# Optimization experiments

Measured on AMD Instinct MI355X. Metric: run time of the kernel, lower is better.

The kernel has to match this reference:

```python
import jax, jax.numpy as jnp
import numpy as np

N = 40000      # nodes (adj.size(0))
ISIZE = 64     # feature dim
K = 24         # kept kNN neighbors per node after d_cut mask
E = N * K      # learner candidate edges
E_ADJ = N * K  # GCN adjacency edges
OMEGA = 0.9
GAMMA = 2.0
D_CUT = 1.5


def setup_inputs() -> dict:
    key = jax.random.key(0)
    k = jax.random.split(key, 8)
    features = jax.random.normal(k[0], (N, ISIZE), jnp.float32)
    sc = 1.0 / np.sqrt(ISIZE)
    W1 = jax.random.normal(k[1], (ISIZE, ISIZE), jnp.float32) * sc
    b1 = jnp.zeros((ISIZE,), jnp.float32)
    W2 = jax.random.normal(k[2], (ISIZE, ISIZE), jnp.float32) * sc
    b2 = jnp.zeros((ISIZE,), jnp.float32)
    adj_row = jax.random.randint(k[3], (E_ADJ,), 0, N, dtype=jnp.int32)
    adj_col = jax.random.randint(k[4], (E_ADJ,), 0, N, dtype=jnp.int32)
    # kNN-style candidate edges: K neighbors per node, no self loops
    i_idx = jnp.repeat(jnp.arange(N, dtype=jnp.int32), K)
    j_idx = (i_idx + jax.random.randint(k[5], (E,), 1, N, dtype=jnp.int32)) % N
    # precomputed distance prior: s_d = 1/exp(gamma*(d/d_cut)^2)
    dist = jax.random.uniform(k[6], (E,), jnp.float32, 0.1, 2.0)
    s_d = jnp.exp(-GAMMA * (dist / D_CUT) ** 2)
    return {"features": features, "W1": W1, "b1": b1, "W2": W2, "b2": b2,
            "s_d": s_d, "adj_row": adj_row, "adj_col": adj_col,
            "i_idx": i_idx, "j_idx": j_idx}


def _gcn(x, W, b, row, col):
    """PyG GCNConv: symmetric norm with self loops, aggregate src=row into dst=col."""
    xw = x @ W
    deg = 1.0 + jax.ops.segment_sum(jnp.ones((row.shape[0],), jnp.float32), col,
                                    num_segments=N)
    dinv = jax.lax.rsqrt(deg)
    msg = (dinv[row] * dinv[col])[:, None] * xw[row]            # [E_ADJ, ISIZE]
    out = jax.ops.segment_sum(msg, col, num_segments=N)
    return out + (dinv * dinv)[:, None] * xw + b                # self-loop + bias


def reference(features, W1, b1, W2, b2, s_d, adj_row, adj_col, i_idx, j_idx):
    # GCN stack (nlayers=2), ReLU between layers
    h = jax.nn.relu(_gcn(features, W1, b1, adj_row, adj_col))
    h = _gcn(h, W2, b2, adj_row, adj_col)
    # F.normalize(h, p=2, dim=-1)
    h = h / jnp.maximum(jnp.linalg.norm(h, axis=-1, keepdims=True), 1e-12)
    # per-edge cosine scores, clamped at 0, blended with distance prior
    s_val = jnp.sum(h[i_idx] * h[j_idx], axis=-1)               # [E]
    s_val = jax.nn.relu(s_val)
    s_val = OMEGA * s_val + (1.0 - OMEGA) * s_d
    # SparseTensor.to_symmetric(reduce='mean'): average with reverse edge if present
    keys = i_idx * N + j_idx                                    # fits int32 (N=4e4)
    rkeys = j_idx * N + i_idx
    order = jnp.argsort(keys)
    sk = keys[order]
    pos = jnp.clip(jnp.searchsorted(sk, rkeys), 0, E - 1)
    found = sk[pos] == rkeys
    rev = order[pos]
    v_sym = jnp.where(found, 0.5 * (s_val + s_val[rev]), s_val)
    # symmetric COO: original edges + reverse copies (zeroed where reverse existed)
    rows_s = jnp.concatenate([i_idx, j_idx])                    # [2E]
    cols_s = jnp.concatenate([j_idx, i_idx])
    vals_s = jnp.concatenate([v_sym, jnp.where(found, 0.0, v_sym)])
    # normalize_adj_symm: D^{-1/2} S D^{-1/2}
    deg = jax.ops.segment_sum(vals_s, rows_s, num_segments=N)
    dinv = jnp.where(deg > 0, jax.lax.rsqrt(jnp.maximum(deg, 1e-12)), 0.0)
    vals_norm = dinv[rows_s] * vals_s * dinv[cols_s]
    return vals_norm, vals_s
```

## Files before the change

kernel.cpp:

```cpp
#include <hip/hip_runtime.h>

#define N_NODES 40000
#define ISIZE   64
#define KNN     24
#define NE      (N_NODES * KNN)
#define OMEGA   0.9f
#define CAP     64
#define NBUCK   80
#define LBUCK   10
#define BCAP    16384
#define JBCAP   16384
#define EPT     8
#define PBCH    512

__device__ __forceinline__ float bf2f(unsigned short s) {
    return __uint_as_float(((unsigned)s) << 16);
}
__device__ __forceinline__ unsigned short f2bf(float f) {
    unsigned u = __float_as_uint(f);
    u += 0x7fffu + ((u >> 16) & 1u);
    return (unsigned short)(u >> 16);
}
__device__ __forceinline__ float bflo(unsigned u) { return __uint_as_float(u << 16); }
__device__ __forceinline__ float bfhi(unsigned u) { return __uint_as_float(u & 0xffff0000u); }
__device__ __forceinline__ unsigned pack2(float lo, float hi) {
    return (unsigned)f2bf(lo) | ((unsigned)f2bf(hi) << 16);
}

__global__ void k_mega1(const float* __restrict__ X, const float* __restrict__ W,
                        unsigned short* __restrict__ Y0, unsigned short* __restrict__ Y1,
                        const int* __restrict__ row, const int* __restrict__ col,
                        const int* __restrict__ j_idx,
                        int* __restrict__ bcnt, unsigned* __restrict__ bbuf,
                        unsigned* __restrict__ ovf2, int* __restrict__ ovf2_cnt,
                        int* __restrict__ jbcnt, unsigned* __restrict__ jbbuf,
                        unsigned* __restrict__ jovf, int* __restrict__ jovf_cnt,
                        unsigned char* __restrict__ revb) {
    __shared__ float sW[64 * 64];
    __shared__ float sX[32 * 64];
    const int GB  = N_NODES / 32;
    const int NBA = (NE + 256 * EPT - 1) / (256 * EPT);
    int bx = blockIdx.x;
    int tid = threadIdx.x;
    if (bx < GB) {
        int row0 = bx * 32;
        for (int t = tid; t < 1024; t += 256)
            ((float4*)sW)[t] = ((const float4*)W)[t];
        for (int t = tid; t < 512; t += 256)
            ((float4*)sX)[t] = ((const float4*)(X + row0 * 64))[t];
        __syncthreads();
        int cc = tid & 63;
        int rl = tid >> 6;
        for (int r = rl; r < 32; r += 4) {
            float acc = 0.0f;
#pragma unroll
            for (int kk = 0; kk < 64; kk++) acc += sX[r * 64 + kk] * sW[kk * 64 + cc];
            if (cc < 32) Y0[(row0 + r) * 32 + cc]      = f2bf(acc);
            else         Y1[(row0 + r) * 32 + cc - 32] = f2bf(acc);
        }
    } else if (bx < GB + 2 * NBA) {
        int* lcnt  = (int*)sW;
        int* lbase = lcnt + NBUCK;
        int blk = bx - GB;
        bool adj = blk < NBA;
        if (!adj) blk -= NBA;
        for (int b = tid; b < NBUCK; b += 256) lcnt[b] = 0;
        __syncthreads();
        int e0 = blk * (256 * EPT);
        int myslot[EPT]; int myb[EPT]; unsigned myp[EPT];
        for (int k = 0; k < EPT; k++) {
            int e = e0 + k * 256 + tid;
            if (e < NE) {
                int b; unsigned p;
                if (adj) { int r = row[e], c = col[e]; b = c >> 9; p = ((unsigned)r << 16) | (unsigned)c; }
                else     { int j = j_idx[e];           b = j >> 9; p = ((unsigned)(j & 511) << 20) | (unsigned)e; }
                myb[k] = b; myp[k] = p;
                myslot[k] = atomicAdd(&lcnt[b], 1);
            } else myb[k] = -1;
        }
        __syncthreads();
        int* gcnt = adj ? bcnt : jbcnt;
        for (int b = tid; b < NBUCK; b += 256)
            lbase[b] = (lcnt[b] > 0) ? atomicAdd(&gcnt[b], lcnt[b]) : 0;
        __syncthreads();
        unsigned* gbuf = adj ? bbuf : jbbuf;
        unsigned* govf = adj ? ovf2 : jovf;
        int* gocnt = adj ? ovf2_cnt : jovf_cnt;
        for (int k = 0; k < EPT; k++) {
            if (myb[k] < 0) continue;
            int pos = lbase[myb[k]] + myslot[k];
            if (pos < BCAP) gbuf[myb[k] * BCAP + pos] = myp[k];
            else { int p = atomicAdd(gocnt, 1); govf[p] = myp[k]; }
        }
    } else {
        int t = (bx - GB - 2 * NBA) * 256 + tid;
        int e = t >> 3;
        int q = t & 7;
        int i = e / KNN;
        int j = j_idx[e];
        const int* jj = j_idx + j * KNN;
        int rt = 255;
        if (jj[q] == i) rt = q;
        if (jj[8 + q] == i) rt = min(rt, 8 + q);
        if (jj[16 + q] == i) rt = min(rt, 16 + q);
#pragma unroll
        for (int m = 1; m < 8; m <<= 1) rt = min(rt, __shfl_xor(rt, m));
        if (q == 0) revb[e] = (unsigned char)rt;
    }
}

__global__ void k_scatter2(const unsigned* __restrict__ bbuf, const int* __restrict__ bcnt,
                           int* __restrict__ cnt, unsigned short* __restrict__ ebuf,
                           unsigned* __restrict__ ovf, int* __restrict__ ovf_cnt,
                           const unsigned* __restrict__ ovf2, const int* __restrict__ ovf2_cnt) {
    const int MAIN = 8 * LBUCK * (BCAP / PBCH);
    if ((int)blockIdx.x >= MAIN) {
        int m = ovf2_cnt[0];
        for (int t = (blockIdx.x - MAIN) * 256 + threadIdx.x; t < m; t += 8 * 256) {
            unsigned p = ovf2[t];
            int c = (int)(p & 0xffffu), r = (int)(p >> 16);
            int slot = atomicAdd(&cnt[c], 1);
            if (slot < CAP) ebuf[c * CAP + slot] = (unsigned short)r;
            else { int q = atomicAdd(ovf_cnt, 1); ovf[q] = p; }
        }
        return;
    }
    int xcd = blockIdx.x & 7;
    int t   = blockIdx.x >> 3;
    int lb  = t % LBUCK;
    int chunk = t / LBUCK;
    int b = xcd + 8 * lb;
    int n = min(bcnt[b], BCAP);
    int start = chunk * PBCH;
    if (start >= n) return;
    int end = min(start + PBCH, n);
    for (int idx = start + threadIdx.x; idx < end; idx += 256) {
        unsigned p = bbuf[b * BCAP + idx];
        int c = (int)(p & 0xffffu), r = (int)(p >> 16);
        int slot = atomicAdd(&cnt[c], 1);
        if (slot < CAP) ebuf[c * CAP + slot] = (unsigned short)r;
        else { int q = atomicAdd(ovf_cnt, 1); ovf[q] = p; }
    }
}

__global__ void k_gemm2(const unsigned short* __restrict__ X, const float* __restrict__ W,
                        unsigned short* __restrict__ Y0, unsigned short* __restrict__ Y1) {
    __shared__ float sW[64 * 64];
    __shared__ float sX[32 * 64];
    int row0 = blockIdx.x * 32;
    for (int t = threadIdx.x; t < 1024; t += 256)
        ((float4*)sW)[t] = ((const float4*)W)[t];
    for (int t = threadIdx.x; t < 512; t += 256) {
        uint2 u = ((const uint2*)(X + row0 * 64))[t];
        ((float4*)sX)[t] = make_float4(bflo(u.x), bfhi(u.x), bflo(u.y), bfhi(u.y));
    }
    __syncthreads();
    int col = threadIdx.x & 63;
    int rl  = threadIdx.x >> 6;
    for (int r = rl; r < 32; r += 4) {
        float acc = 0.0f;
#pragma unroll
        for (int kk = 0; kk < 64; kk++) acc += sX[r * 64 + kk] * sW[kk * 64 + col];
        if (col < 32) Y0[(row0 + r) * 32 + col]      = f2bf(acc);
        else          Y1[(row0 + r) * 32 + col - 32] = f2bf(acc);
    }
}

template<bool RELU, bool NORM>
__global__ void k_aggf4(const uint4* __restrict__ X0q, const uint4* __restrict__ X1q,
                        uint4* __restrict__ outFq,
                        uint4* __restrict__ O0q, uint4* __restrict__ O1q,
                        const int* __restrict__ cnt,
                        const unsigned short* __restrict__ ebuf, const float* __restrict__ bias,
                        const unsigned* __restrict__ ovf, const int* __restrict__ ovf_cnt) {
    int w = (blockIdx.x * 256 + threadIdx.x) >> 6;
    int lane = threadIdx.x & 63;
    int half = lane >> 5, sl = lane & 31;
    int n = w * 2 + half;
    if (n >= N_NODES) return;
    int deg = cnt[n];
    int bucketed = min(deg, CAP);
    int nb0 = min(bucketed, 32);
    int nb1 = bucketed - nb0;

    int   r0v = 0, r1v = 0;
    float d0v = 0.0f, d1v = 0.0f;
    if (sl < nb0) { r0v = (int)ebuf[n * CAP + sl];      d0v = rsqrtf(1.0f + (float)cnt[r0v]); }
    if (sl < nb1) { r1v = (int)ebuf[n * CAP + 32 + sl]; d1v = rsqrtf(1.0f + (float)cnt[r1v]); }

    int g = sl >> 2;
    int f = sl & 3;

    float a[16];
#pragma unroll
    for (int k = 0; k < 16; k++) a[k] = 0.f;

    int np0 = (nb0 + 7) >> 3;
    int np1 = (nb1 + 7) >> 3;

#pragma unroll 4
    for (int d = 0; d < np0; d++) {
        int   q = 8 * d + g;
        int   r = __shfl(r0v, q, 32);
        float c = __shfl(d0v, q, 32);
        uint4 u0 = X0q[r * 4 + f];
        uint4 u1 = X1q[r * 4 + f];
        a[0]  += c * bflo(u0.x); a[1]  += c * bfhi(u0.x);
        a[2]  += c * bflo(u0.y); a[3]  += c * bfhi(u0.y);
        a[4]  += c * bflo(u0.z); a[5]  += c * bfhi(u0.z);
        a[6]  += c * bflo(u0.w); a[7]  += c * bfhi(u0.w);
        a[8]  += c * bflo(u1.x); a[9]  += c * bfhi(u1.x);
        a[10] += c * bflo(u1.y); a[11] += c * bfhi(u1.y);
        a[12] += c * bflo(u1.z); a[13] += c * bfhi(u1.z);
        a[14] += c * bflo(u1.w); a[15] += c * bfhi(u1.w);
    }
#pragma unroll 4
    for (int d = 0; d < np1; d++) {
        int   q = 8 * d + g;
        int   r = __shfl(r1v, q, 32);
        float c = __shfl(d1v, q, 32);
        uint4 u0 = X0q[r * 4 + f];
        uint4 u1 = X1q[r * 4 + f];
        a[0]  += c * bflo(u0.x); a[1]  += c * bfhi(u0.x);
        a[2]  += c * bflo(u0.y); a[3]  += c * bfhi(u0.y);
        a[4]  += c * bflo(u0.z); a[5]  += c * bfhi(u0.z);
        a[6]  += c * bflo(u0.w); a[7]  += c * bfhi(u0.w);
        a[8]  += c * bflo(u1.x); a[9]  += c * bfhi(u1.x);
        a[10] += c * bflo(u1.y); a[11] += c * bfhi(u1.y);
        a[12] += c * bflo(u1.z); a[13] += c * bfhi(u1.z);
        a[14] += c * bflo(u1.w); a[15] += c * bfhi(u1.w);
    }

    if (deg > CAP) {
        int m = ovf_cnt[0];
        for (int k2 = 0; k2 < m; k2++) {
            unsigned p = ovf[k2];
            if ((int)(p & 0xffffu) == n && g == 0) {
                int r = (int)(p >> 16);
                float c = rsqrtf(1.0f + (float)cnt[r]);
                uint4 u0 = X0q[r * 4 + f], u1 = X1q[r * 4 + f];
                a[0]  += c * bflo(u0.x); a[1]  += c * bfhi(u0.x);
                a[2]  += c * bflo(u0.y); a[3]  += c * bfhi(u0.y);
                a[4]  += c * bflo(u0.z); a[5]  += c * bfhi(u0.z);
                a[6]  += c * bflo(u0.w); a[7]  += c * bfhi(u0.w);
                a[8]  += c * bflo(u1.x); a[9]  += c * bfhi(u1.x);
                a[10] += c * bflo(u1.y); a[11] += c * bfhi(u1.y);
                a[12] += c * bflo(u1.z); a[13] += c * bfhi(u1.z);
                a[14] += c * bflo(u1.w); a[15] += c * bfhi(u1.w);
            }
        }
    }

#pragma unroll
    for (int k = 0; k < 16; k++) {
        a[k] += __shfl_xor(a[k], 4, 32);
        a[k] += __shfl_xor(a[k], 8, 32);
        a[k] += __shfl_xor(a[k], 16, 32);
    }

    float di = rsqrtf(1.0f + (float)deg);
    float dd = di * di;
    uint4 s0 = X0q[n * 4 + f], s1 = X1q[n * 4 + f];
    float4 bA0 = ((const float4*)bias)[2 * f];
    float4 bA1 = ((const float4*)bias)[2 * f + 1];
    float4 bB0 = ((const float4*)(bias + 32))[2 * f];
    float4 bB1 = ((const float4*)(bias + 32))[2 * f + 1];
    float v[16];
    v[0]  = di * a[0]  + dd * bflo(s0.x) + bA0.x;
    v[1]  = di * a[1]  + dd * bfhi(s0.x) + bA0.y;
    v[2]  = di * a[2]  + dd * bflo(s0.y) + bA0.z;
    v[3]  = di * a[3]  + dd * bfhi(s0.y) + bA0.w;
    v[4]  = di * a[4]  + dd * bflo(s0.z) + bA1.x;
    v[5]  = di * a[5]  + dd * bfhi(s0.z) + bA1.y;
    v[6]  = di * a[6]  + dd * bflo(s0.w) + bA1.z;
    v[7]  = di * a[7]  + dd * bfhi(s0.w) + bA1.w;
    v[8]  = di * a[8]  + dd * bflo(s1.x) + bB0.x;
    v[9]  = di * a[9]  + dd * bfhi(s1.x) + bB0.y;
    v[10] = di * a[10] + dd * bflo(s1.y) + bB0.z;
    v[11] = di * a[11] + dd * bfhi(s1.y) + bB0.w;
    v[12] = di * a[12] + dd * bflo(s1.z) + bB1.x;
    v[13] = di * a[13] + dd * bfhi(s1.z) + bB1.y;
    v[14] = di * a[14] + dd * bflo(s1.w) + bB1.z;
    v[15] = di * a[15] + dd * bfhi(s1.w) + bB1.w;
    if (RELU) {
#pragma unroll
        for (int k = 0; k < 16; k++) v[k] = fmaxf(v[k], 0.f);
    }
    if (NORM) {
        float s = 0.f;
#pragma unroll
        for (int k = 0; k < 16; k++) s += v[k] * v[k];
        s += __shfl_xor(s, 1, 32);
        s += __shfl_xor(s, 2, 32);
        float inv = 1.0f / fmaxf(sqrtf(s), 1e-12f);
#pragma unroll
        for (int k = 0; k < 16; k++) v[k] *= inv;
        if (g == 0) {
            O0q[n * 4 + f] = make_uint4(pack2(v[0], v[1]),  pack2(v[2], v[3]),
                                        pack2(v[4], v[5]),  pack2(v[6], v[7]));
            O1q[n * 4 + f] = make_uint4(pack2(v[8], v[9]),  pack2(v[10], v[11]),
                                        pack2(v[12], v[13]), pack2(v[14], v[15]));
        }
    } else {
        if (g == 0) {
            outFq[n * 8 + f]     = make_uint4(pack2(v[0], v[1]),  pack2(v[2], v[3]),
                                              pack2(v[4], v[5]),  pack2(v[6], v[7]));
            outFq[n * 8 + 4 + f] = make_uint4(pack2(v[8], v[9]),  pack2(v[10], v[11]),
                                              pack2(v[12], v[13]), pack2(v[14], v[15]));
        }
    }
}

__global__ void k_dotsym(const uint4* __restrict__ H0q, const uint4* __restrict__ H1q,
                         const float* __restrict__ s_d, const int* __restrict__ j_idx,
                         const unsigned char* __restrict__ revb,
                         float* __restrict__ outS) {
    int t = blockIdx.x * 256 + threadIdx.x;
    int e = t >> 3;
    int q = t & 7;
    int g = q >> 2, f = q & 3;
    int i = e / KNN;
    int j = j_idx[e];
    int node = g ? j : i;
    uint4 u0 = H0q[node * 4 + f];
    uint4 u1 = H1q[node * 4 + f];
    uint4 p0, p1;
    p0.x = __shfl_xor(u0.x, 4); p0.y = __shfl_xor(u0.y, 4);
    p0.z = __shfl_xor(u0.z, 4); p0.w = __shfl_xor(u0.w, 4);
    p1.x = __shfl_xor(u1.x, 4); p1.y = __shfl_xor(u1.y, 4);
    p1.z = __shfl_xor(u1.z, 4); p1.w = __shfl_xor(u1.w, 4);
    float s = bflo(u0.x) * bflo(p0.x) + bfhi(u0.x) * bfhi(p0.x)
            + bflo(u0.y) * bflo(p0.y) + bfhi(u0.y) * bfhi(p0.y)
            + bflo(u0.z) * bflo(p0.z) + bfhi(u0.z) * bfhi(p0.z)
            + bflo(u0.w) * bflo(p0.w) + bfhi(u0.w) * bfhi(p0.w)
            + bflo(u1.x) * bflo(p1.x) + bfhi(u1.x) * bfhi(p1.x)
            + bflo(u1.y) * bflo(p1.y) + bfhi(u1.y) * bfhi(p1.y)
            + bflo(u1.z) * bflo(p1.z) + bfhi(u1.z) * bfhi(p1.z)
            + bflo(u1.w) * bflo(p1.w) + bfhi(u1.w) * bfhi(p1.w);
    s += __shfl_xor(s, 1);
    s += __shfl_xor(s, 2);
    if (q == 0) {
        float base = OMEGA * fmaxf(s, 0.0f);
        int rt = revb[e];
        float vv, v2;
        if (rt != 255) {
            int rev = j * KNN + rt;
            vv = base + 0.5f * (1.0f - OMEGA) * (s_d[e] + s_d[rev]);
            v2 = 0.0f;
        } else {
            vv = base + (1.0f - OMEGA) * s_d[e];
            v2 = vv;
        }
        outS[e] = vv;
        outS[NE + e] = v2;
    }
}

__global__ void k_jagg(const unsigned* __restrict__ jbbuf, const int* __restrict__ jbcnt,
                       const float* __restrict__ outS, float* __restrict__ dinv2,
                       const unsigned* __restrict__ jovf, const int* __restrict__ jovf_cnt,
                       const int* __restrict__ j_idx) {
    __shared__ float ld[512];
    int b = blockIdx.x;
    int tid = threadIdx.x;
    if (tid < 512) ld[tid] = 0.0f;
    __syncthreads();
    const float* outSv2 = outS + NE;
    int n = min(jbcnt[b], JBCAP);
    for (int idx = tid; idx < n; idx += 1024) {
        unsigned p = jbbuf[b * JBCAP + idx];
        atomicAdd(&ld[p >> 20], outSv2[p & 0xFFFFFu]);
    }
    int m = jovf_cnt[0];
    for (int t2 = tid; t2 < m; t2 += 1024) {
        int e = (int)(jovf[t2] & 0xFFFFFu);
        int j = j_idx[e];
        if ((j >> 9) == b) atomicAdd(&ld[j & 511], outSv2[e]);
    }
    __syncthreads();
    if (tid < 512) {
        int node = b * 512 + tid;
        if (node < N_NODES) {
            float d = ld[tid];
            const float* pp = outS + node * KNN;
#pragma unroll
            for (int qq = 0; qq < KNN; qq++) d += pp[qq];
            dinv2[node] = (d > 0.0f) ? rsqrtf(fmaxf(d, 1e-12f)) : 0.0f;
        }
    }
}

__global__ void k_norm(const float* __restrict__ outS, const float* __restrict__ dinv2,
                       const int* __restrict__ j_idx, float* __restrict__ out) {
    int t = blockIdx.x * 256 + threadIdx.x;
    int r, c;
    if (t < NE) { r = t / KNN; c = j_idx[t]; }
    else        { int e = t - NE; r = j_idx[e]; c = e / KNN; }
    out[t] = dinv2[r] * outS[t] * dinv2[c];
}

extern "C" void kernel_launch(void* const* d_in, const int* in_sizes, int n_in,
                              void* d_out, int out_size, void* d_ws, size_t ws_size,
                              hipStream_t stream) {
    const float* features = (const float*)d_in[0];
    const float* W1       = (const float*)d_in[1];
    const float* b1       = (const float*)d_in[2];
    const float* W2       = (const float*)d_in[3];
    const float* b2       = (const float*)d_in[4];
    const float* s_d      = (const float*)d_in[5];
    const int*   adj_row  = (const int*)d_in[6];
    const int*   adj_col  = (const int*)d_in[7];
    const int*   j_idx    = (const int*)d_in[9];
    float* out = (float*)d_out;

    const int N64 = N_NODES * 64;
    const int N32 = N_NODES * 32;
    int*   cnt     = (int*)d_ws;
    int*   ovfcnts = cnt + N_NODES;
    int*   bcnt    = ovfcnts + 16;
    int*   jbcnt   = bcnt + NBUCK;
    float* dinv2   = (float*)(jbcnt + NBUCK);
    unsigned short* A0  = (unsigned short*)(dinv2 + N_NODES);
    unsigned short* A1  = A0 + N32;
    unsigned short* B16 = A1 + N32;
    unsigned short* H0  = B16 + N64;
    unsigned short* H1  = H0 + N32;
    unsigned short* ebuf = H1 + N32;
    unsigned* ovf    = (unsigned*)(ebuf + N_NODES * CAP);
    unsigned char* revb = (unsigned char*)(ovf + NE);
    unsigned* bbuf   = (unsigned*)(revb + NE);
    unsigned* jbbuf  = bbuf + NBUCK * BCAP;
    unsigned* ovf2   = jbbuf + NBUCK * JBCAP;
    unsigned* jovf   = ovf2 + NE;

    size_t zero_bytes = (size_t)(N_NODES + 16 + 2 * NBUCK) * 4;
    hipMemsetAsync(cnt, 0, zero_bytes, stream);

    const int GB = N_NODES / 32;
    const int NBA = (NE + 256 * EPT - 1) / (256 * EPT);
    const int RB = NE * 8 / 256;
    k_mega1<<<GB + 2 * NBA + RB, 256, 0, stream>>>(
        features, W1, A0, A1, adj_row, adj_col, j_idx,
        bcnt, bbuf, ovf2, ovfcnts + 4, jbcnt, jbbuf, jovf, ovfcnts + 8, revb);

    k_scatter2<<<8 * LBUCK * (BCAP / PBCH) + 8, 256, 0, stream>>>(
        bbuf, bcnt, cnt, ebuf, ovf, ovfcnts, ovf2, ovfcnts + 4);

    k_aggf4<true, false><<<(N_NODES / 2 * 64 + 255) / 256, 256, 0, stream>>>(
        (const uint4*)A0, (const uint4*)A1, (uint4*)B16, nullptr, nullptr,
        cnt, ebuf, b1, ovf, ovfcnts);

    k_gemm2<<<N_NODES / 32, 256, 0, stream>>>(B16, W2, A0, A1);
    k_aggf4<false, true><<<(N_NODES / 2 * 64 + 255) / 256, 256, 0, stream>>>(
        (const uint4*)A0, (const uint4*)A1, nullptr, (uint4*)H0, (uint4*)H1,
        cnt, ebuf, b2, ovf, ovfcnts);

    float* outS = out + 2 * NE;
    k_dotsym<<<NE * 8 / 256, 256, 0, stream>>>(
        (const uint4*)H0, (const uint4*)H1, s_d, j_idx, revb, outS);

    k_jagg<<<NBUCK, 1024, 0, stream>>>(jbbuf, jbcnt, outS, dinv2, jovf, ovfcnts + 8, j_idx);
    k_norm<<<2 * NE / 256, 256, 0, stream>>>(outS, dinv2, j_idx, out);
}
```

Before: 271.6 us.

## Scatter adjacency per bucket with shared-memory counters; vectorize reverse-edge lookup

The adjacency scatter kernel now runs one 1024-thread block per destination bucket of 512 nodes. Slot counters live in shared-memory atomics instead of global ones, and the final counts are written to global memory once per node. Each block also filters the shared overflow list for its own bucket, so every block rescans the whole overflow list. The reverse-edge search now uses one thread per edge that reads the 24 neighbors as six uint4 loads, replacing eight cooperating threads and a shuffle reduction. This trades global atomic traffic and block count for fewer, larger blocks with less parallelism.

```diff
diff --git a/kernel.cpp b/kernel.cpp
--- a/kernel.cpp
+++ b/kernel.cpp
@@ -7,11 +7,9 @@
 #define OMEGA   0.9f
 #define CAP     64
 #define NBUCK   80
-#define LBUCK   10
 #define BCAP    16384
 #define JBCAP   16384
 #define EPT     8
-#define PBCH    512
 
 __device__ __forceinline__ float bf2f(unsigned short s) {
     return __uint_as_float(((unsigned)s) << 16);
@@ -93,53 +91,53 @@
             else { int p = atomicAdd(gocnt, 1); govf[p] = myp[k]; }
         }
     } else {
-        int t = (bx - GB - 2 * NBA) * 256 + tid;
-        int e = t >> 3;
-        int q = t & 7;
+        int e = (bx - GB - 2 * NBA) * 256 + tid;
         int i = e / KNN;
         int j = j_idx[e];
-        const int* jj = j_idx + j * KNN;
+        const uint4* jj4 = (const uint4*)(j_idx + j * KNN);
         int rt = 255;
-        if (jj[q] == i) rt = q;
-        if (jj[8 + q] == i) rt = min(rt, 8 + q);
-        if (jj[16 + q] == i) rt = min(rt, 16 + q);
-#pragma unroll
-        for (int m = 1; m < 8; m <<= 1) rt = min(rt, __shfl_xor(rt, m));
-        if (q == 0) revb[e] = (unsigned char)rt;
-    }
-}
-
-__global__ void k_scatter2(const unsigned* __restrict__ bbuf, const int* __restrict__ bcnt,
+#pragma unroll
+        for (int k = 5; k >= 0; k--) {
+            uint4 u = jj4[k];
+            if ((int)u.w == i) rt = 4 * k + 3;
+            if ((int)u.z == i) rt = 4 * k + 2;
+            if ((int)u.y == i) rt = 4 * k + 1;
+            if ((int)u.x == i) rt = 4 * k + 0;
+        }
+        revb[e] = (unsigned char)rt;
+    }
+}
+
+__global__ void k_scatter3(const unsigned* __restrict__ bbuf, const int* __restrict__ bcnt,
                            int* __restrict__ cnt, unsigned short* __restrict__ ebuf,
                            unsigned* __restrict__ ovf, int* __restrict__ ovf_cnt,
                            const unsigned* __restrict__ ovf2, const int* __restrict__ ovf2_cnt) {
-    const int MAIN = 8 * LBUCK * (BCAP / PBCH);
-    if ((int)blockIdx.x >= MAIN) {
-        int m = ovf2_cnt[0];
-        for (int t = (blockIdx.x - MAIN) * 256 + threadIdx.x; t < m; t += 8 * 256) {
-            unsigned p = ovf2[t];
-            int c = (int)(p & 0xffffu), r = (int)(p >> 16);
-            int slot = atomicAdd(&cnt[c], 1);
-            if (slot < CAP) ebuf[c * CAP + slot] = (unsigned short)r;
-            else { int q = atomicAdd(ovf_cnt, 1); ovf[q] = p; }
-        }
-        return;
-    }
-    int xcd = blockIdx.x & 7;
-    int t   = blockIdx.x >> 3;
-    int lb  = t % LBUCK;
-    int chunk = t / LBUCK;
-    int b = xcd + 8 * lb;
+    __shared__ int lcnt2[512];
+    int b = blockIdx.x;
+    int tid = threadIdx.x;
+    if (tid < 512) lcnt2[tid] = 0;
+    __syncthreads();
     int n = min(bcnt[b], BCAP);
-    int start = chunk * PBCH;
-    if (start >= n) return;
-    int end = min(start + PBCH, n);
-    for (int idx = start + threadIdx.x; idx < end; idx += 256) {
+    for (int idx = tid; idx < n; idx += 1024) {
         unsigned p = bbuf[b * BCAP + idx];
         int c = (int)(p & 0xffffu), r = (int)(p >> 16);
-        int slot = atomicAdd(&cnt[c], 1);
+        int slot = atomicAdd(&lcnt2[c & 511], 1);
         if (slot < CAP) ebuf[c * CAP + slot] = (unsigned short)r;
         else { int q = atomicAdd(ovf_cnt, 1); ovf[q] = p; }
+    }
+    int m = ovf2_cnt[0];
+    for (int idx = tid; idx < m; idx += 1024) {
+        unsigned p = ovf2[idx];
+        int c = (int)(p & 0xffffu), r = (int)(p >> 16);
+        if ((c >> 9) != b) continue;
+        int slot = atomicAdd(&lcnt2[c & 511], 1);
+        if (slot < CAP) ebuf[c * CAP + slot] = (unsigned short)r;
+        else { int q = atomicAdd(ovf_cnt, 1); ovf[q] = p; }
+    }
+    __syncthreads();
+    if (tid < 512) {
+        int node = b * 512 + tid;
+        if (node < N_NODES) cnt[node] = lcnt2[tid];
     }
 }
 
@@ -438,13 +436,13 @@
 
     const int GB = N_NODES / 32;
     const int NBA = (NE + 256 * EPT - 1) / (256 * EPT);
-    const int RB = NE * 8 / 256;
+    const int RB = NE / 256;
     k_mega1<<<GB + 2 * NBA + RB, 256, 0, stream>>>(
         features, W1, A0, A1, adj_row, adj_col, j_idx,
         bcnt, bbuf, ovf2, ovfcnts + 4, jbcnt, jbbuf, jovf, ovfcnts + 8, revb);
 
-    k_scatter2<<<8 * LBUCK * (BCAP / PBCH) + 8, 256, 0, stream>>>(
-        bbuf, bcnt, cnt, ebuf, ovf, ovfcnts, ovf2, ovfcnts + 4);
+    k_scatter3<<<NBUCK, 1024, 0, stream>>>(bbuf, bcnt, cnt, ebuf,
+                                           ovf, ovfcnts, ovf2, ovfcnts + 4);
 
     k_aggf4<true, false><<<(N_NODES / 2 * 64 + 255) / 256, 256, 0, stream>>>(
         (const uint4*)A0, (const uint4*)A1, (uint4*)B16, nullptr, nullptr,
```

New measurement: 252.0 us. 1.08x faster.
